# Performance work log

Measured on AMD Instinct MI355X. Metric: run time of the kernel, lower is better.

Reference implementation:

```python
import jax, jax.numpy as jnp
import numpy as np

TEMPERATURE = 0.07


def setup_inputs() -> dict:
    key = jax.random.key(0)
    k1, k2 = jax.random.split(key)
    B, D = 8192, 1024
    emb1 = jax.random.normal(k1, (B, D), dtype=jnp.float32)
    emb2 = jax.random.normal(k2, (B, D), dtype=jnp.float32)
    return {"emb1": emb1, "emb2": emb2}


def reference(emb1, emb2):
    B = emb1.shape[0]
    # [B, B] similarity logits scaled by temperature
    logits = jnp.matmul(emb1, emb2.T) / TEMPERATURE
    # SigLIP-style contrastive loss: diagonal entries are positives,
    # off-diagonal entries are negatives.
    # positive: -logsigmoid(logits) on diag; negative: -logsigmoid(-logits) off-diag
    pos = -jax.nn.log_sigmoid(jnp.diagonal(logits))            # [B]
    neg = -jax.nn.log_sigmoid(-logits)                          # [B, B]
    # negative_mask zeroes the diagonal -> subtract diagonal contribution
    neg_sum = neg.sum() - jnp.sum(jnp.diagonal(neg))
    loss = (pos.sum() + neg_sum) / B
    return loss
```

## Files before the change

kernel.cpp:

```cpp
#include <hip/hip_runtime.h>


#define B_DIM 8192
#define K_DIM 1024
#define BT 128
#define BKB 128
#define NT (K_DIM / BKB)
#define BRICK 16384
#define PANEL_BYTES (NT * BRICK)
#define BUFSZ 32768

typedef int i32x4 __attribute__((ext_vector_type(4)));
typedef int i32x8 __attribute__((ext_vector_type(8)));
typedef float f32x4 __attribute__((ext_vector_type(4)));

__device__ __forceinline__ void brick_store(const float* __restrict__ in,
                                            unsigned char* __restrict__ out,
                                            float scale, int i) {
  const int o = i * 16;
  const int b = o >> 14;
  const int p = b >> 3, t = b & 7;
  const int w = o & (BRICK - 1);
  const int fb = w >> 11;
  const int h = (w >> 10) & 1;
  const int kch = (w >> 8) & 3;
  const int lr = (w >> 4) & 15;
  const int row = p * 128 + fb * 16 + lr;
  const int kb = t * 128 + kch * 32 + h * 16;
  const float4* src = (const float4*)(in + (size_t)row * K_DIM + kb);
  float4 v0 = src[0], v1 = src[1], v2 = src[2], v3 = src[3];
  unsigned w0 = 0, w1 = 0, w2 = 0, w3 = 0;
  w0 = __builtin_amdgcn_cvt_pk_fp8_f32(v0.x * scale, v0.y * scale, w0, 0);
  w0 = __builtin_amdgcn_cvt_pk_fp8_f32(v0.z * scale, v0.w * scale, w0, 1);
  w1 = __builtin_amdgcn_cvt_pk_fp8_f32(v1.x * scale, v1.y * scale, w1, 0);
  w1 = __builtin_amdgcn_cvt_pk_fp8_f32(v1.z * scale, v1.w * scale, w1, 1);
  w2 = __builtin_amdgcn_cvt_pk_fp8_f32(v2.x * scale, v2.y * scale, w2, 0);
  w2 = __builtin_amdgcn_cvt_pk_fp8_f32(v2.z * scale, v2.w * scale, w2, 1);
  w3 = __builtin_amdgcn_cvt_pk_fp8_f32(v3.x * scale, v3.y * scale, w3, 0);
  w3 = __builtin_amdgcn_cvt_pk_fp8_f32(v3.z * scale, v3.w * scale, w3, 1);
  *(uint4*)(out + o) = make_uint4(w0, w1, w2, w3);
}

__global__ __launch_bounds__(256) void cvt_fused(
    const float* __restrict__ e1, const float* __restrict__ e2,
    unsigned char* __restrict__ A8, unsigned char* __restrict__ B8,
    int nbA, float scaleA) {
  const int blk = blockIdx.x;
  if (blk < nbA)
    brick_store(e1, A8, scaleA, blk * 256 + threadIdx.x);
  else
    brick_store(e2, B8, 1.0f, (blk - nbA) * 256 + threadIdx.x);
}

template <bool DIAG>
__device__ __forceinline__ float softplus_sum(const f32x4 (&acc)[4][4],
                                              int rbase, int cbase) {
  float lin = 0.f, cor = 0.f;
#pragma unroll
  for (int m = 0; m < 4; ++m) {
#pragma unroll
    for (int n = 0; n < 4; ++n) {
#pragma unroll
      for (int r = 0; r < 4; ++r) {
        float x = acc[m][n][r];
        if (DIAG) {
          int row = rbase + m * 16 + r;
          int col = cbase + n * 16;
          if (row == col) x = -x;
        }
        lin += fmaxf(x, 0.f);
        cor += __logf(1.f + __expf(-fabsf(x)));
      }
    }
  }
  return lin + cor;
}

#define STAGEA(SB, Q, TI)                                                     \
  __builtin_amdgcn_global_load_lds(                                           \
      (const __attribute__((address_space(1))) void*)(const void*)(           \
          srcA + (TI) * BRICK + (Q) * 1024),                                  \
      (__attribute__((address_space(3))) void*)(void*)(                       \
          lds + (SB) + dA + (Q) * 1024),                                      \
      16, 0, 0)
#define STAGEB(SB, Q, TI)                                                     \
  __builtin_amdgcn_global_load_lds(                                           \
      (const __attribute__((address_space(1))) void*)(const void*)(           \
          srcB + (TI) * BRICK + (Q) * 1024),                                  \
      (__attribute__((address_space(3))) void*)(void*)(                       \
          lds + (SB) + dB + (Q) * 1024),                                      \
      16, 0, 0)

#define LDA(OUT, RB, M)                                                       \
  {                                                                           \
    const unsigned char* _b = ldsL + ((RB) + ((wr * 4 + (M)) << 11));         \
    i32x4 _lo = *(const i32x4*)(_b);                                          \
    i32x4 _hi = *(const i32x4*)(_b + 1024);                                   \
    OUT = __builtin_shufflevector(_lo, _hi, 0, 1, 2, 3, 4, 5, 6, 7);          \
  }
#define LDB(OUT, RB, N)                                                       \
  {                                                                           \
    const unsigned char* _b = ldsL + ((RB) + 16384 + ((wc * 4 + (N)) << 11)); \
    i32x4 _lo = *(const i32x4*)(_b);                                          \
    i32x4 _hi = *(const i32x4*)(_b + 1024);                                   \
    OUT = __builtin_shufflevector(_lo, _hi, 0, 1, 2, 3, 4, 5, 6, 7);          \
  }

#define MFMA(AF, BF, M, N)                                                    \
  acc[M][N] = __builtin_amdgcn_mfma_scale_f32_16x16x128_f8f6f4(               \
      AF, BF, acc[M][N], 0, 0, 0, 127, 0, 127)

__global__ __launch_bounds__(256, 2) void siglip_gemm(
    const unsigned char* __restrict__ A8,
    const unsigned char* __restrict__ B8,
    float* __restrict__ partials) {
  __shared__ unsigned char lds[2 * BUFSZ];
  __shared__ float wsum[4];

  const int tid = threadIdx.x;
  const int wave = tid >> 6;
  const int lane = tid & 63;
  const int wr = wave >> 1;
  const int wc = wave & 1;
  const int brow = blockIdx.y;
  const int bcol = blockIdx.x;

  f32x4 acc[4][4];
#pragma unroll
  for (int m = 0; m < 4; ++m)
#pragma unroll
    for (int n = 0; n < 4; ++n) acc[m][n] = f32x4{0.f, 0.f, 0.f, 0.f};

  const unsigned char* srcA =
      A8 + (size_t)brow * PANEL_BYTES + wave * 4096 + (lane << 4);
  const unsigned char* srcB =
      B8 + (size_t)bcol * PANEL_BYTES + wave * 4096 + (lane << 4);
  const int dA = wave * 4096;
  const int dB = 16384 + wave * 4096;
  const unsigned char* ldsL = lds + (lane << 4);

  STAGEA(0, 0, 0); STAGEA(0, 1, 0); STAGEA(0, 2, 0); STAGEA(0, 3, 0);
  STAGEB(0, 0, 0); STAGEB(0, 1, 0); STAGEB(0, 2, 0); STAGEB(0, 3, 0);
  asm volatile("s_waitcnt vmcnt(0)" ::: "memory");
  __builtin_amdgcn_s_barrier();
  __builtin_amdgcn_sched_barrier(0);

#pragma unroll
  for (int T = 0; T < NT; ++T) {
    const int rb = (T & 1) * BUFSZ;
    const int sb = rb ^ BUFSZ;

    i32x8 b0, b1, b2, b3, a0, a1, a2, a3;
    LDB(b0, rb, 0); LDB(b1, rb, 1); LDB(b2, rb, 2); LDB(b3, rb, 3);
    LDA(a0, rb, 0); LDA(a1, rb, 1); LDA(a2, rb, 2); LDA(a3, rb, 3);

    if (T < NT - 1) {
      STAGEA(sb, 0, T + 1); STAGEA(sb, 1, T + 1);
      STAGEA(sb, 2, T + 1); STAGEA(sb, 3, T + 1);
      STAGEB(sb, 0, T + 1); STAGEB(sb, 1, T + 1);
      STAGEB(sb, 2, T + 1); STAGEB(sb, 3, T + 1);
    }
    __builtin_amdgcn_sched_barrier(0);

    __builtin_amdgcn_s_setprio(1);
    MFMA(a0, b0, 0, 0); MFMA(a0, b1, 0, 1); MFMA(a0, b2, 0, 2); MFMA(a0, b3, 0, 3);
    MFMA(a1, b0, 1, 0); MFMA(a1, b1, 1, 1); MFMA(a1, b2, 1, 2); MFMA(a1, b3, 1, 3);
    MFMA(a2, b0, 2, 0); MFMA(a2, b1, 2, 1); MFMA(a2, b2, 2, 2); MFMA(a2, b3, 2, 3);
    MFMA(a3, b0, 3, 0); MFMA(a3, b1, 3, 1); MFMA(a3, b2, 3, 2); MFMA(a3, b3, 3, 3);
    __builtin_amdgcn_s_setprio(0);

    if (T < NT - 1) {
      asm volatile("s_waitcnt vmcnt(0)" ::: "memory");
      __builtin_amdgcn_s_barrier();
      __builtin_amdgcn_sched_barrier(0);
    }
  }

  const int rbase = brow * BT + wr * 64 + (lane >> 4) * 4;
  const int cbase = bcol * BT + wc * 64 + (lane & 15);
  float lsum;
  if (brow == bcol)
    lsum = softplus_sum<true>(acc, rbase, cbase);
  else
    lsum = softplus_sum<false>(acc, rbase, cbase);

#pragma unroll
  for (int off = 32; off > 0; off >>= 1) lsum += __shfl_down(lsum, off);
  __syncthreads();
  if (lane == 0) wsum[wave] = lsum;
  __syncthreads();
  if (tid == 0)
    partials[blockIdx.y * gridDim.x + blockIdx.x] =
        wsum[0] + wsum[1] + wsum[2] + wsum[3];
}

__global__ void reduce_kernel(const float* __restrict__ partials, int n,
                              float* __restrict__ out) {
  __shared__ float s[256];
  float v = 0.f;
  for (int i = threadIdx.x; i < n; i += 256) v += partials[i];
  s[threadIdx.x] = v;
  __syncthreads();
  for (int off = 128; off > 0; off >>= 1) {
    if ((int)threadIdx.x < off) s[threadIdx.x] += s[threadIdx.x + off];
    __syncthreads();
  }
  if (threadIdx.x == 0) out[0] = s[0] / (float)B_DIM;
}

extern "C" void kernel_launch(void* const* d_in, const int* in_sizes, int n_in,
                              void* d_out, int out_size, void* d_ws, size_t ws_size,
                              hipStream_t stream) {
  const float* emb1 = (const float*)d_in[0];
  const float* emb2 = (const float*)d_in[1];

  unsigned char* A8 = (unsigned char*)d_ws;
  unsigned char* B8 = A8 + (size_t)B_DIM * K_DIM;
  float* partials = (float*)(B8 + (size_t)B_DIM * K_DIM);

  const float INV_T = 1.0f / 0.07f;
  const int nbA = (B_DIM * K_DIM / 16) / 256;
  cvt_fused<<<2 * nbA, 256, 0, stream>>>(emb1, emb2, A8, B8, nbA, INV_T);

  dim3 grid(B_DIM / BT, B_DIM / BT);
  siglip_gemm<<<grid, 256, 0, stream>>>(A8, B8, partials);

  const int nparts = (B_DIM / BT) * (B_DIM / BT);
  reduce_kernel<<<1, 256, 0, stream>>>(partials, nparts, (float*)d_out);
}
```

Before: 113.6 us.

## Enlarge GEMM block tile to 256x256 with 16 waves per block

Each block now covers a 256x256 output tile with 1024 threads arranged as a 4x4 grid of waves, each still computing a 64x64 sub-tile. The LDS staging buffers double to 128 KB total and every wave stages one 4 KB slice of the four A/B panels. This halves global/L2 traffic per output element through more reuse, and there are four times fewer partials. In exchange, only one block fits per CU, the grid drops to 1024 blocks, and the barriers now synchronise 16 waves, which may hurt latency hiding.

New measurement: 250.3 us. 120% more time.

```diff
diff --git a/kernel.cpp b/kernel.cpp
--- a/kernel.cpp
+++ b/kernel.cpp
@@ -3,12 +3,12 @@
 
 #define B_DIM 8192
 #define K_DIM 1024
-#define BT 128
+#define BT 256
 #define BKB 128
 #define NT (K_DIM / BKB)
 #define BRICK 16384
 #define PANEL_BYTES (NT * BRICK)
-#define BUFSZ 32768
+#define BUFSZ 65536
 
 typedef int i32x4 __attribute__((ext_vector_type(4)));
 typedef int i32x8 __attribute__((ext_vector_type(8)));
@@ -76,31 +76,24 @@
   return lin + cor;
 }
 
-#define STAGEA(SB, Q, TI)                                                     \
+#define STAGE(SB, Q, TI)                                                      \
   __builtin_amdgcn_global_load_lds(                                           \
       (const __attribute__((address_space(1))) void*)(const void*)(           \
-          srcA + (TI) * BRICK + (Q) * 1024),                                  \
+          srcP + (TI) * BRICK + (Q) * 1024),                                  \
       (__attribute__((address_space(3))) void*)(void*)(                       \
-          lds + (SB) + dA + (Q) * 1024),                                      \
-      16, 0, 0)
-#define STAGEB(SB, Q, TI)                                                     \
-  __builtin_amdgcn_global_load_lds(                                           \
-      (const __attribute__((address_space(1))) void*)(const void*)(           \
-          srcB + (TI) * BRICK + (Q) * 1024),                                  \
-      (__attribute__((address_space(3))) void*)(void*)(                       \
-          lds + (SB) + dB + (Q) * 1024),                                      \
+          lds + (SB) + dstoff + (Q) * 1024),                                  \
       16, 0, 0)
 
 #define LDA(OUT, RB, M)                                                       \
   {                                                                           \
-    const unsigned char* _b = ldsL + ((RB) + ((wr * 4 + (M)) << 11));         \
+    const unsigned char* _b = ldsL + ((RB) + aoff + ((M) << 11));             \
     i32x4 _lo = *(const i32x4*)(_b);                                          \
     i32x4 _hi = *(const i32x4*)(_b + 1024);                                   \
     OUT = __builtin_shufflevector(_lo, _hi, 0, 1, 2, 3, 4, 5, 6, 7);          \
   }
 #define LDB(OUT, RB, N)                                                       \
   {                                                                           \
-    const unsigned char* _b = ldsL + ((RB) + 16384 + ((wc * 4 + (N)) << 11)); \
+    const unsigned char* _b = ldsL + ((RB) + boff + ((N) << 11));             \
     i32x4 _lo = *(const i32x4*)(_b);                                          \
     i32x4 _hi = *(const i32x4*)(_b + 1024);                                   \
     OUT = __builtin_shufflevector(_lo, _hi, 0, 1, 2, 3, 4, 5, 6, 7);          \
@@ -110,18 +103,18 @@
   acc[M][N] = __builtin_amdgcn_mfma_scale_f32_16x16x128_f8f6f4(               \
       AF, BF, acc[M][N], 0, 0, 0, 127, 0, 127)
 
-__global__ __launch_bounds__(256, 2) void siglip_gemm(
+__global__ __launch_bounds__(1024, 1) void siglip_gemm(
     const unsigned char* __restrict__ A8,
     const unsigned char* __restrict__ B8,
     float* __restrict__ partials) {
   __shared__ unsigned char lds[2 * BUFSZ];
-  __shared__ float wsum[4];
+  __shared__ float wsum[16];
 
   const int tid = threadIdx.x;
   const int wave = tid >> 6;
   const int lane = tid & 63;
-  const int wr = wave >> 1;
-  const int wc = wave & 1;
+  const int wr = wave >> 2;
+  const int wc = wave & 3;
   const int brow = blockIdx.y;
   const int bcol = blockIdx.x;
 
@@ -131,16 +124,19 @@
 #pragma unroll
     for (int n = 0; n < 4; ++n) acc[m][n] = f32x4{0.f, 0.f, 0.f, 0.f};
 
-  const unsigned char* srcA =
-      A8 + (size_t)brow * PANEL_BYTES + wave * 4096 + (lane << 4);
-  const unsigned char* srcB =
-      B8 + (size_t)bcol * PANEL_BYTES + wave * 4096 + (lane << 4);
-  const int dA = wave * 4096;
-  const int dB = 16384 + wave * 4096;
+  const int sreg = wave >> 2;
+  const int ssub = wave & 3;
+  const unsigned char* srcP =
+      (sreg < 2 ? A8 + (size_t)(2 * brow + sreg) * PANEL_BYTES
+                : B8 + (size_t)(2 * bcol + (sreg - 2)) * PANEL_BYTES) +
+      ssub * 4096 + (lane << 4);
+  const int dstoff = sreg * 16384 + ssub * 4096;
+
+  const int aoff = (wr >> 1) * 16384 + ((wr & 1) * 4) * 2048;
+  const int boff = 32768 + (wc >> 1) * 16384 + ((wc & 1) * 4) * 2048;
   const unsigned char* ldsL = lds + (lane << 4);
 
-  STAGEA(0, 0, 0); STAGEA(0, 1, 0); STAGEA(0, 2, 0); STAGEA(0, 3, 0);
-  STAGEB(0, 0, 0); STAGEB(0, 1, 0); STAGEB(0, 2, 0); STAGEB(0, 3, 0);
+  STAGE(0, 0, 0); STAGE(0, 1, 0); STAGE(0, 2, 0); STAGE(0, 3, 0);
   asm volatile("s_waitcnt vmcnt(0)" ::: "memory");
   __builtin_amdgcn_s_barrier();
   __builtin_amdgcn_sched_barrier(0);
@@ -155,10 +151,8 @@
     LDA(a0, rb, 0); LDA(a1, rb, 1); LDA(a2, rb, 2); LDA(a3, rb, 3);
 
     if (T < NT - 1) {
-      STAGEA(sb, 0, T + 1); STAGEA(sb, 1, T + 1);
-      STAGEA(sb, 2, T + 1); STAGEA(sb, 3, T + 1);
-      STAGEB(sb, 0, T + 1); STAGEB(sb, 1, T + 1);
-      STAGEB(sb, 2, T + 1); STAGEB(sb, 3, T + 1);
+      STAGE(sb, 0, T + 1); STAGE(sb, 1, T + 1);
+      STAGE(sb, 2, T + 1); STAGE(sb, 3, T + 1);
     }
     __builtin_amdgcn_sched_barrier(0);
 
@@ -189,9 +183,12 @@
   __syncthreads();
   if (lane == 0) wsum[wave] = lsum;
   __syncthreads();
-  if (tid == 0)
-    partials[blockIdx.y * gridDim.x + blockIdx.x] =
-        wsum[0] + wsum[1] + wsum[2] + wsum[3];
+  if (tid == 0) {
+    float s = 0.f;
+#pragma unroll
+    for (int w = 0; w < 16; ++w) s += wsum[w];
+    partials[blockIdx.y * gridDim.x + blockIdx.x] = s;
+  }
 }
 
 __global__ void reduce_kernel(const float* __restrict__ partials, int n,
@@ -223,7 +220,7 @@
   cvt_fused<<<2 * nbA, 256, 0, stream>>>(emb1, emb2, A8, B8, nbA, INV_T);
 
   dim3 grid(B_DIM / BT, B_DIM / BT);
-  siglip_gemm<<<grid, 256, 0, stream>>>(A8, B8, partials);
+  siglip_gemm<<<grid, 1024, 0, stream>>>(A8, B8, partials);
 
   const int nparts = (B_DIM / BT) * (B_DIM / BT);
   reduce_kernel<<<1, 256, 0, stream>>>(partials, nparts, (float*)d_out);
```
